# Kernel tuning notes

Measured on AMD Instinct MI355X. Metric: run time of the kernel, lower is better.

Reference implementation:

```python
import jax, jax.numpy as jnp
import numpy as np

B, N, IN_DIM, L_DIM, H_DIM, N_CLASSES, FLOW_LEN = 128, 512, 128, 64, 64, 10, 4


def setup_inputs() -> dict:
    key = jax.random.key(0)
    ks = jax.random.split(key, 20)
    s = 0.05
    return {
        "gs": jax.random.uniform(ks[0], (B, N, N), dtype=jnp.float32),
        "hs": jax.random.normal(ks[1], (B, N, IN_DIM), dtype=jnp.float32),
        "labels": jax.random.randint(ks[2], (B,), 0, N_CLASSES),
        "eps": jax.random.normal(ks[3], (B, N, 1), dtype=jnp.float32),
        "W_s": jax.random.normal(ks[4], (IN_DIM, L_DIM), dtype=jnp.float32) * s,
        "b_s": jnp.zeros((L_DIM,), jnp.float32),
        "W_mu": jax.random.normal(ks[5], (L_DIM, 1), dtype=jnp.float32) * s,
        "b_mu": jnp.zeros((1,), jnp.float32),
        "W_lv": jax.random.normal(ks[6], (L_DIM, 1), dtype=jnp.float32) * s,
        "b_lv": jnp.zeros((1,), jnp.float32),
        "W_dec": jax.random.normal(ks[7], (1, L_DIM), dtype=jnp.float32) * s,
        "b_dec": jnp.zeros((L_DIM,), jnp.float32),
        "W1": jax.random.normal(ks[8], (L_DIM, H_DIM), dtype=jnp.float32) * s,
        "b1": jnp.zeros((H_DIM,), jnp.float32),
        "W2": jax.random.normal(ks[9], (H_DIM, N_CLASSES), dtype=jnp.float32) * s,
        "b2": jnp.zeros((N_CLASSES,), jnp.float32),
        "beta": jax.random.uniform(ks[10], (1,), jnp.float32, 0.0, 100.0),
        "fw": jax.random.normal(ks[11], (FLOW_LEN,), dtype=jnp.float32) * 0.1,
        "fb": jax.random.normal(ks[12], (FLOW_LEN,), dtype=jnp.float32) * 0.1,
        "fs": jax.random.normal(ks[13], (FLOW_LEN,), dtype=jnp.float32) * 0.1,
    }


def reference(gs, hs, labels, eps, W_s, b_s, W_mu, b_mu, W_lv, b_lv,
              W_dec, b_dec, W1, b1, W2, b2, beta, fw, fb, fs):
    relu = jax.nn.relu
    # norm_g: g / g.sum(1) (torch broadcast divides column j by row-sum deg[j])
    deg = gs.sum(axis=2)                       # [B, N]
    g = gs / deg[:, None, :]                   # [B, N, N]

    def gcn(g, h, W, b):
        return relu(jnp.einsum('bij,bjf->bif', g, h) @ W + b)

    h = gcn(g, hs, W_s, b_s)                   # [B, N, L]
    r = h
    mu = gcn(g, h, W_mu, b_mu)                 # [B, N, 1]
    logvar = gcn(g, h, W_lv, b_lv)             # [B, N, 1]
    sigma = jnp.exp(0.5 * logvar)
    z0 = eps * sigma + mu                      # reparameterize (training)

    # 4-step planar flow on scalar latent; log-det accumulated on pre-transform z
    z = z0
    log_jac = jnp.zeros_like(z0)
    for k in range(FLOW_LEN):
        t = jnp.tanh(fw[k] * z + fb[k])
        det = 1.0 + fs[k] * fw[k] * (1.0 - t * t)
        log_jac = log_jac + jnp.log(jnp.abs(det) + 1e-7)
        z = z + fs[k] * t
    zk = z

    # KL = log q(z0) - log_jac - log p(zk), loggaussian = -0.5*((z-mu)/s)^2 - log(2.5 s)
    logq = -0.5 * ((z0 - mu) / sigma) ** 2 - jnp.log(2.5 * sigma)
    logp = -0.5 * zk ** 2 - jnp.log(jnp.float32(2.5))
    kl = logq - log_jac - logp                 # [B, N, 1]

    zs = jax.nn.sigmoid(beta * zk)             # [B, N, 1]
    d = gcn(g, zs, W_dec, b_dec)               # [B, N, L]
    hg = jnp.einsum('bnl,bn->bl', h, zs[..., 0])  # h.T @ zk, [B, L]

    # classify
    x = relu(hg @ W1 + b1)
    logits = jax.nn.log_softmax(x @ W2 + b2, axis=1)  # [B, C]

    nll = -jnp.mean(logits[jnp.arange(B), labels])
    mse = jnp.mean((r - d) ** 2)
    loss = nll + mse + kl.mean()
    preds = jnp.argmax(logits, axis=1)
    acc = jnp.mean((preds == labels).astype(jnp.float32))
    return jnp.stack([loss, acc])
```

## Files before the change

### kernel.cpp

```cpp
#include <hip/hip_runtime.h>
#include <hip/hip_bf16.h>

#define BB 128
#define NN 512
#define IND 128
#define LD 64
#define NC 10
#define FL 4
#define ROWS (BB*NN)
#define HALF 256

#define OFF_ACC 0
#define OFF_RDEG (OFF_ACC + 8)
#define OFF_VM   (OFF_RDEG + ROWS)
#define OFF_VV   (OFF_VM + ROWS)
#define OFF_ZS   (OFF_VV + ROWS)
#define OFF_ZSS  (OFF_ZS + ROWS)
#define OFF_XHG  (OFF_ZSS + ROWS)
#define OFF_H    (OFF_XHG + BB*128)
#define OFF_GSB  (OFF_H + ROWS*32)
#define WS_NEED ((size_t)(OFF_GSB + (size_t)ROWS*256) * 4)

typedef __attribute__((ext_vector_type(8))) short short8v;
typedef __attribute__((ext_vector_type(4))) float f32x4;

__device__ inline float wave_reduce(float v) {
    #pragma unroll
    for (int m = 32; m; m >>= 1) v += __shfl_xor(v, m, 64);
    return v;
}

__device__ inline short f2bf(float f) {
    unsigned u = __float_as_uint(f);
    u += 0x7fff + ((u >> 16) & 1);
    return (short)(u >> 16);
}

__device__ inline float bf2f(short s) {
    return __uint_as_float(((unsigned)(unsigned short)s) << 16);
}

__global__ __launch_bounds__(256) void k_deg(const float* __restrict__ gs,
                                             float* __restrict__ rdeg,
                                             float* __restrict__ accums,
                                             unsigned short* __restrict__ gsb) {
    if (blockIdx.x == 0 && threadIdx.x < 8) accums[threadIdx.x] = 0.f;
    int t = threadIdx.x;
    int row = blockIdx.x * 4 + (t >> 6), lane = t & 63;
    const float4* r4 = (const float4*)(gs + (size_t)row * NN) + lane * 2;
    float4 a = r4[0], b = r4[1];
    float s = a.x + a.y + a.z + a.w + b.x + b.y + b.z + b.w;
    float sr = wave_reduce(s);
    if (lane == 0) rdeg[row] = 1.0f / sr;
    if (gsb) {
        short8v v;
        v[0] = f2bf(a.x); v[1] = f2bf(a.y); v[2] = f2bf(a.z); v[3] = f2bf(a.w);
        v[4] = f2bf(b.x); v[5] = f2bf(b.y); v[6] = f2bf(b.z); v[7] = f2bf(b.w);
        *(short8v*)(gsb + (size_t)row * NN + lane * 8) = v;
    }
}

template<bool BF>
__global__ __launch_bounds__(1024) void k_hwgemm(
    const float* __restrict__ gs, const unsigned short* __restrict__ gsb,
    const float* __restrict__ hs, const float* __restrict__ W_s,
    const float* __restrict__ b_s, const float* __restrict__ W_mu,
    const float* __restrict__ W_lv, const float* __restrict__ rdeg_ws,
    unsigned short* __restrict__ h_ws, float* __restrict__ vm_ws,
    float* __restrict__ vv_ws)
{
    __shared__ unsigned short s_hwT[64 * 512];
    __shared__ unsigned short s_h[HALF * 64];
    __shared__ float s_rdeg[NN];

    const int tid = threadIdx.x, lane = tid & 63, wid = tid >> 6;
    const int b = blockIdx.x >> 1, p = blockIdx.x & 1, rbase = p * HALF;

    if (tid < NN) s_rdeg[tid] = rdeg_ws[(size_t)b * NN + tid];

    unsigned short* sWT = s_h;
    {
        const float4* wp = (const float4*)W_s + tid * 2;
        float4 w0 = wp[0], w1 = wp[1];
        int k = tid >> 3, l0 = (tid & 7) * 8;
        float wv[8] = {w0.x, w0.y, w0.z, w0.w, w1.x, w1.y, w1.z, w1.w};
        #pragma unroll
        for (int e = 0; e < 8; ++e) {
            int l = l0 + e;
            int byte = (l * 256 + k * 2) ^ ((l & 7) << 4);
            *(unsigned short*)((char*)sWT + byte) = (unsigned short)f2bf(wv[e]);
        }
    }
    __syncthreads();

    {
        int n0 = wid * 32, cq = lane & 15, koq = lane >> 4;
        f32x4 accB[2][4] = {};
        #pragma unroll
        for (int kk = 0; kk < 4; ++kk) {
            short8v bf[4];
            #pragma unroll
            for (int lt = 0; lt < 4; ++lt) {
                int l = lt * 16 + cq;
                int byte = (l * 256 + (kk * 32 + koq * 8) * 2) ^ ((l & 7) << 4);
                bf[lt] = *(const short8v*)((char*)sWT + byte);
            }
            #pragma unroll
            for (int nt = 0; nt < 2; ++nt) {
                int row = n0 + nt * 16 + cq;
                const float4* hp = (const float4*)(hs + ((size_t)b * NN + row) * IND
                                                   + kk * 32 + koq * 8);
                float4 h0 = hp[0], h1 = hp[1];
                short8v a;
                a[0] = f2bf(h0.x); a[1] = f2bf(h0.y); a[2] = f2bf(h0.z); a[3] = f2bf(h0.w);
                a[4] = f2bf(h1.x); a[5] = f2bf(h1.y); a[6] = f2bf(h1.z); a[7] = f2bf(h1.w);
                #pragma unroll
                for (int lt = 0; lt < 4; ++lt)
                    accB[nt][lt] = __builtin_amdgcn_mfma_f32_16x16x32_bf16(a, bf[lt], accB[nt][lt], 0, 0, 0);
            }
        }
        __syncthreads();
        int r0 = (lane >> 4) * 4;
        #pragma unroll
        for (int nt = 0; nt < 2; ++nt)
            #pragma unroll
            for (int lt = 0; lt < 4; ++lt)
                #pragma unroll
                for (int q = 0; q < 4; ++q) {
                    int n = n0 + nt * 16 + r0 + q;
                    int l = lt * 16 + cq;
                    int byte = (l * 1024 + n * 2) ^ ((l & 7) << 4);
                    *(unsigned short*)((char*)s_hwT + byte) =
                        (unsigned short)f2bf(accB[nt][lt][q] * s_rdeg[n]);
                }
    }
    __syncthreads();

    {
        int cq = lane & 15, koq = lane >> 4;
        int rowl = wid * 16 + cq, rowg = rbase + rowl;
        const unsigned short* A16 = gsb + ((size_t)b * NN + rowg) * NN + koq * 8;
        const float* A32 = gs + ((size_t)b * NN + rowg) * NN + koq * 8;
        f32x4 accC[4] = {};
        for (int kk = 0; kk < 16; ++kk) {
            short8v bf[4];
            #pragma unroll
            for (int lt = 0; lt < 4; ++lt) {
                int l = lt * 16 + cq;
                int byte = (l * 1024 + (kk * 32 + koq * 8) * 2) ^ ((l & 7) << 4);
                bf[lt] = *(const short8v*)((char*)s_hwT + byte);
            }
            short8v a;
            if constexpr (BF) {
                a = *(const short8v*)(A16 + kk * 32);
            } else {
                const float4* gp = (const float4*)(A32 + kk * 32);
                float4 g0 = gp[0], g1 = gp[1];
                a[0] = f2bf(g0.x); a[1] = f2bf(g0.y); a[2] = f2bf(g0.z); a[3] = f2bf(g0.w);
                a[4] = f2bf(g1.x); a[5] = f2bf(g1.y); a[6] = f2bf(g1.z); a[7] = f2bf(g1.w);
            }
            #pragma unroll
            for (int lt = 0; lt < 4; ++lt)
                accC[lt] = __builtin_amdgcn_mfma_f32_16x16x32_bf16(a, bf[lt], accC[lt], 0, 0, 0);
        }
        int r0 = (lane >> 4) * 4;
        float bsv[4];
        #pragma unroll
        for (int lt = 0; lt < 4; ++lt) bsv[lt] = b_s[lt * 16 + cq];
        #pragma unroll
        for (int lt = 0; lt < 4; ++lt)
            #pragma unroll
            for (int q = 0; q < 4; ++q) {
                int nloc = wid * 16 + r0 + q;
                int l = lt * 16 + cq;
                s_h[nloc * 64 + l] = (unsigned short)f2bf(fmaxf(accC[lt][q] + bsv[lt], 0.f));
            }
    }
    __syncthreads();

    {
        int rowl = tid >> 2, off = (tid & 3) * 16;
        unsigned short* dst = h_ws + ((size_t)(b * NN + rbase + rowl)) * 64 + off;
        const unsigned short* src = &s_h[rowl * 64 + off];
        *(short8v*)dst = *(const short8v*)src;
        *(short8v*)(dst + 8) = *(const short8v*)(src + 8);
    }

    {
        int g16 = tid >> 4, l16 = tid & 15;
        float wmu[4], wlv[4];
        #pragma unroll
        for (int e = 0; e < 4; ++e) { wmu[e] = W_mu[l16 * 4 + e]; wlv[e] = W_lv[l16 * 4 + e]; }
        #pragma unroll
        for (int rr = 0; rr < 4; ++rr) {
            int rowl = g16 * 4 + rr;
            const unsigned short* hp = &s_h[rowl * 64 + l16 * 4];
            float pm = 0.f, pv = 0.f;
            #pragma unroll
            for (int e = 0; e < 4; ++e) {
                float hv = bf2f((short)hp[e]);
                pm += hv * wmu[e]; pv += hv * wlv[e];
            }
            #pragma unroll
            for (int m = 1; m <= 8; m <<= 1) {
                pm += __shfl_xor(pm, m, 64);
                pv += __shfl_xor(pv, m, 64);
            }
            if (l16 == 0) {
                float rd = s_rdeg[rbase + rowl];
                vm_ws[(size_t)b * NN + rbase + rowl] = pm * rd;
                vv_ws[(size_t)b * NN + rbase + rowl] = pv * rd;
            }
        }
    }
}

template<bool BF>
__global__ __launch_bounds__(1024) void k_muflow(
    const float* __restrict__ gs, const unsigned short* __restrict__ gsb,
    const float* __restrict__ vm_ws, const float* __restrict__ vv_ws,
    const float* __restrict__ eps, const float* __restrict__ b_mu,
    const float* __restrict__ b_lv, const float* __restrict__ beta,
    const float* __restrict__ fw, const float* __restrict__ fb,
    const float* __restrict__ fs, const float* __restrict__ rdeg_ws,
    float* __restrict__ zs_ws, float* __restrict__ zss_ws,
    float* __restrict__ accums)
{
    __shared__ float s_mp[HALF], s_lp[HALF];
    __shared__ float s_fin[16];
    const int tid = threadIdx.x, lane = tid & 63, wid = tid >> 6;
    const int b = blockIdx.x >> 1, p = blockIdx.x & 1, rbase = p * HALF;

    float vmr[8], vvr[8];
    #pragma unroll
    for (int e = 0; e < 8; ++e) {
        vmr[e] = vm_ws[(size_t)b * NN + lane * 8 + e];
        vvr[e] = vv_ws[(size_t)b * NN + lane * 8 + e];
    }
    for (int r = 0; r < 16; ++r) {
        int rowl = wid * 16 + r, rowg = rbase + rowl;
        float sm, sv;
        if constexpr (BF) {
            short8v g8 = *(const short8v*)(gsb + ((size_t)b * NN + rowg) * NN + lane * 8);
            float g0 = bf2f(g8[0]), g1 = bf2f(g8[1]), g2 = bf2f(g8[2]), g3 = bf2f(g8[3]);
            float g4 = bf2f(g8[4]), g5 = bf2f(g8[5]), g6 = bf2f(g8[6]), g7 = bf2f(g8[7]);
            sm = g0*vmr[0]+g1*vmr[1]+g2*vmr[2]+g3*vmr[3]+g4*vmr[4]+g5*vmr[5]+g6*vmr[6]+g7*vmr[7];
            sv = g0*vvr[0]+g1*vvr[1]+g2*vvr[2]+g3*vvr[3]+g4*vvr[4]+g5*vvr[5]+g6*vvr[6]+g7*vvr[7];
        } else {
            const float4* gp = (const float4*)(gs + ((size_t)b * NN + rowg) * NN) + lane * 2;
            float4 ga = gp[0], gc = gp[1];
            sm = ga.x*vmr[0]+ga.y*vmr[1]+ga.z*vmr[2]+ga.w*vmr[3]
               + gc.x*vmr[4]+gc.y*vmr[5]+gc.z*vmr[6]+gc.w*vmr[7];
            sv = ga.x*vvr[0]+ga.y*vvr[1]+ga.z*vvr[2]+ga.w*vvr[3]
               + gc.x*vvr[4]+gc.y*vvr[5]+gc.z*vvr[6]+gc.w*vvr[7];
        }
        sm = wave_reduce(sm);
        sv = wave_reduce(sv);
        if (lane == 0) { s_mp[rowl] = sm; s_lp[rowl] = sv; }
    }
    __syncthreads();

    float my_kl = 0.f;
    if (tid < HALF) {
        int rowg = rbase + tid;
        float mu = fmaxf(s_mp[tid] + b_mu[0], 0.f);
        float lv = fmaxf(s_lp[tid] + b_lv[0], 0.f);
        float sigma = expf(0.5f * lv);
        float z0 = eps[(size_t)b * NN + rowg] * sigma + mu;
        float z = z0, lj = 0.f;
        #pragma unroll
        for (int k = 0; k < FL; ++k) {
            float tt = tanhf(fw[k] * z + fb[k]);
            float det = 1.f + fs[k] * fw[k] * (1.f - tt * tt);
            lj += logf(fabsf(det) + 1e-7f);
            z += fs[k] * tt;
        }
        float e0 = (z0 - mu) / sigma;
        float logq = -0.5f * e0 * e0 - logf(2.5f * sigma);
        float logp = -0.5f * z * z - logf(2.5f);
        my_kl = logq - lj - logp;
        float zv = 1.f / (1.f + expf(-beta[0] * z));
        float rd = rdeg_ws[(size_t)b * NN + rowg];
        zs_ws[(size_t)b * NN + rowg] = zv;
        zss_ws[(size_t)b * NN + rowg] = zv * rd;
    }
    float kv = wave_reduce(my_kl);
    if (lane == 0) s_fin[wid] = kv;
    __syncthreads();
    if (tid == 0) {
        float ks = 0.f;
        #pragma unroll
        for (int w = 0; w < 16; ++w) ks += s_fin[w];
        atomicAdd(&accums[0], ks);
    }
}

template<bool BF>
__global__ __launch_bounds__(1024) void k_dec(
    const float* __restrict__ gs, const unsigned short* __restrict__ gsb,
    const float* __restrict__ zss_ws, const float* __restrict__ zs_ws,
    const unsigned short* __restrict__ h_ws, const float* __restrict__ W_dec,
    const float* __restrict__ b_dec, float* __restrict__ accums,
    float* __restrict__ xhg)
{
    __shared__ float s_zs[HALF];
    __shared__ float s_red[16 * 68];
    __shared__ float s_fin[16];
    const int tid = threadIdx.x, lane = tid & 63, wid = tid >> 6;
    const int b = blockIdx.x >> 1, p = blockIdx.x & 1, rbase = p * HALF;

    if (tid < HALF) s_zs[tid] = zs_ws[(size_t)b * NN + rbase + tid];
    float zr[8];
    #pragma unroll
    for (int e = 0; e < 8; ++e) zr[e] = zss_ws[(size_t)b * NN + lane * 8 + e];
    float wd = W_dec[lane], bd = b_dec[lane];
    __syncthreads();

    float msacc = 0.f, hgacc = 0.f;
    for (int r = 0; r < 16; ++r) {
        int rowl = wid * 16 + r, rowg = rbase + rowl;
        float s;
        if constexpr (BF) {
            short8v g8 = *(const short8v*)(gsb + ((size_t)b * NN + rowg) * NN + lane * 8);
            s = bf2f(g8[0])*zr[0]+bf2f(g8[1])*zr[1]+bf2f(g8[2])*zr[2]+bf2f(g8[3])*zr[3]
              + bf2f(g8[4])*zr[4]+bf2f(g8[5])*zr[5]+bf2f(g8[6])*zr[6]+bf2f(g8[7])*zr[7];
        } else {
            const float4* gp = (const float4*)(gs + ((size_t)b * NN + rowg) * NN) + lane * 2;
            float4 ga = gp[0], gc = gp[1];
            s = ga.x*zr[0]+ga.y*zr[1]+ga.z*zr[2]+ga.w*zr[3]
              + gc.x*zr[4]+gc.y*zr[5]+gc.z*zr[6]+gc.w*zr[7];
        }
        s = wave_reduce(s);
        float dval = fmaxf(s * wd + bd, 0.f);
        float hval = bf2f((short)h_ws[((size_t)b * NN + rowg) * 64 + lane]);
        float diff = hval - dval;
        msacc += diff * diff;
        hgacc += hval * s_zs[rowl];
    }
    s_red[wid * 68 + lane] = hgacc;
    float mv = wave_reduce(msacc);
    if (lane == 0) s_fin[wid] = mv;
    __syncthreads();
    if (tid == 0) {
        float ms = 0.f;
        #pragma unroll
        for (int w = 0; w < 16; ++w) ms += s_fin[w];
        atomicAdd(&accums[1], ms);
    }
    if (wid == 0) {
        float hgv = 0.f;
        #pragma unroll
        for (int w = 0; w < 16; ++w) hgv += s_red[w * 68 + lane];
        xhg[(size_t)b * 128 + p * 64 + lane] = hgv;
    }
}

__global__ __launch_bounds__(64) void k_cls(const float* __restrict__ xhg,
                                            const float* __restrict__ W1,
                                            const float* __restrict__ b1,
                                            const float* __restrict__ W2,
                                            const float* __restrict__ b2,
                                            const int* __restrict__ labels,
                                            float* __restrict__ accums,
                                            float* __restrict__ out)
{
    __shared__ float s_hg[64], s_x[64], s_lg[12];
    int b = blockIdx.x, l = threadIdx.x;
    s_hg[l] = xhg[(size_t)b * 128 + l] + xhg[(size_t)b * 128 + 64 + l];
    __syncthreads();
    float x = b1[l];
    #pragma unroll 8
    for (int k = 0; k < LD; ++k) x += s_hg[k] * W1[k * LD + l];
    s_x[l] = fmaxf(x, 0.f);
    __syncthreads();
    if (l < NC) {
        float lg = b2[l];
        #pragma unroll 8
        for (int k = 0; k < LD; ++k) lg += s_x[k] * W2[k * NC + l];
        s_lg[l] = lg;
    }
    __syncthreads();
    if (l == 0) {
        float mx = s_lg[0]; int pred = 0;
        #pragma unroll
        for (int c = 1; c < NC; ++c) if (s_lg[c] > mx) { mx = s_lg[c]; pred = c; }
        float se = 0.f;
        #pragma unroll
        for (int c = 0; c < NC; ++c) se += expf(s_lg[c] - mx);
        int lab = labels[b];
        atomicAdd(&accums[2], -(s_lg[lab] - (mx + logf(se))));
        if (pred == lab) atomicAdd(&accums[3], 1.0f);
        __threadfence();
        unsigned old = atomicAdd((unsigned*)&accums[4], 1u);
        if (old == BB - 1) {
            float kk = atomicAdd(&accums[0], 0.f);
            float mm = atomicAdd(&accums[1], 0.f);
            float nn = atomicAdd(&accums[2], 0.f);
            float aa = atomicAdd(&accums[3], 0.f);
            out[0] = nn / (float)BB
                   + mm / ((float)BB * NN * LD)
                   + kk / ((float)BB * NN);
            out[1] = aa / (float)BB;
        }
    }
}

extern "C" void kernel_launch(void* const* d_in, const int* in_sizes, int n_in,
                              void* d_out, int out_size, void* d_ws, size_t ws_size,
                              hipStream_t stream) {
    const float* gs    = (const float*)d_in[0];
    const float* hs    = (const float*)d_in[1];
    const int*   labels= (const int*)d_in[2];
    const float* eps   = (const float*)d_in[3];
    const float* W_s   = (const float*)d_in[4];
    const float* b_s   = (const float*)d_in[5];
    const float* W_mu  = (const float*)d_in[6];
    const float* b_mu  = (const float*)d_in[7];
    const float* W_lv  = (const float*)d_in[8];
    const float* b_lv  = (const float*)d_in[9];
    const float* W_dec = (const float*)d_in[10];
    const float* b_dec = (const float*)d_in[11];
    const float* W1    = (const float*)d_in[12];
    const float* b1    = (const float*)d_in[13];
    const float* W2    = (const float*)d_in[14];
    const float* b2    = (const float*)d_in[15];
    const float* beta  = (const float*)d_in[16];
    const float* fw    = (const float*)d_in[17];
    const float* fb    = (const float*)d_in[18];
    const float* fs    = (const float*)d_in[19];

    float* ws      = (float*)d_ws;
    float* accums  = ws + OFF_ACC;
    float* rdeg    = ws + OFF_RDEG;
    float* vm_ws   = ws + OFF_VM;
    float* vv_ws   = ws + OFF_VV;
    float* zs_ws   = ws + OFF_ZS;
    float* zss_ws  = ws + OFF_ZSS;
    float* xhg     = ws + OFF_XHG;
    unsigned short* h_ws = (unsigned short*)(ws + OFF_H);
    unsigned short* gsb  = (unsigned short*)(ws + OFF_GSB);
    float* out = (float*)d_out;

    bool big = ws_size >= WS_NEED;

    k_deg<<<ROWS / 4, 256, 0, stream>>>(gs, rdeg, accums, big ? gsb : nullptr);
    if (big) {
        k_hwgemm<true><<<2 * BB, 1024, 0, stream>>>(gs, gsb, hs, W_s, b_s, W_mu, W_lv,
                                                    rdeg, h_ws, vm_ws, vv_ws);
        k_muflow<true><<<2 * BB, 1024, 0, stream>>>(gs, gsb, vm_ws, vv_ws, eps, b_mu, b_lv,
                                                    beta, fw, fb, fs, rdeg, zs_ws, zss_ws,
                                                    accums);
        k_dec<true><<<2 * BB, 1024, 0, stream>>>(gs, gsb, zss_ws, zs_ws, h_ws, W_dec, b_dec,
                                                 accums, xhg);
    } else {
        k_hwgemm<false><<<2 * BB, 1024, 0, stream>>>(gs, gsb, hs, W_s, b_s, W_mu, W_lv,
                                                     rdeg, h_ws, vm_ws, vv_ws);
        k_muflow<false><<<2 * BB, 1024, 0, stream>>>(gs, gsb, vm_ws, vv_ws, eps, b_mu, b_lv,
                                                     beta, fw, fb, fs, rdeg, zs_ws, zss_ws,
                                                     accums);
        k_dec<false><<<2 * BB, 1024, 0, stream>>>(gs, gsb, zss_ws, zs_ws, h_ws, W_dec, b_dec,
                                                  accums, xhg);
    }
    k_cls<<<BB, 64, 0, stream>>>(xhg, W1, b1, W2, b2, labels, accums, out);
}
```

Measured before the change: 103.6 us.

## Use bf16 MFMA for mu/logvar and decoder matvecs, split rows into quarters

Replaces the per-row wave-reduced scalar dot products in k_muflow and k_dec with 16x16x32 bf16 MFMA instructions. The vector operands are converted to bf16 and staged in shared memory. Grid goes from 2 to 4 blocks per graph with 512 threads each. Per-block atomics for KL and MSE become per-block partial writes that k_cls sums. This removes the shuffle-reduction cost and adds parallelism, but it rounds the vectors to bf16 and wastes most MFMA columns because they are zero-padded.

```diff
diff --git a/kernel.cpp b/kernel.cpp
--- a/kernel.cpp
+++ b/kernel.cpp
@@ -9,6 +9,7 @@
 #define FL 4
 #define ROWS (BB*NN)
 #define HALF 256
+#define QTR 128
 
 #define OFF_ACC 0
 #define OFF_RDEG (OFF_ACC + 8)
@@ -16,8 +17,10 @@
 #define OFF_VV   (OFF_VM + ROWS)
 #define OFF_ZS   (OFF_VV + ROWS)
 #define OFF_ZSS  (OFF_ZS + ROWS)
-#define OFF_XHG  (OFF_ZSS + ROWS)
-#define OFF_H    (OFF_XHG + BB*128)
+#define OFF_KLP  (OFF_ZSS + ROWS)
+#define OFF_MSEP (OFF_KLP + 512)
+#define OFF_XHG  (OFF_MSEP + 512)
+#define OFF_H    (OFF_XHG + BB*256)
 #define OFF_GSB  (OFF_H + ROWS*32)
 #define WS_NEED ((size_t)(OFF_GSB + (size_t)ROWS*256) * 4)
 
@@ -216,7 +219,7 @@
 }
 
 template<bool BF>
-__global__ __launch_bounds__(1024) void k_muflow(
+__global__ __launch_bounds__(512) void k_muflow(
     const float* __restrict__ gs, const unsigned short* __restrict__ gsb,
     const float* __restrict__ vm_ws, const float* __restrict__ vv_ws,
     const float* __restrict__ eps, const float* __restrict__ b_mu,
@@ -224,49 +227,59 @@
     const float* __restrict__ fw, const float* __restrict__ fb,
     const float* __restrict__ fs, const float* __restrict__ rdeg_ws,
     float* __restrict__ zs_ws, float* __restrict__ zss_ws,
-    float* __restrict__ accums)
+    float* __restrict__ klp)
 {
-    __shared__ float s_mp[HALF], s_lp[HALF];
-    __shared__ float s_fin[16];
+    __shared__ unsigned short s_bmu[NN], s_blv[NN];
+    __shared__ float s_mp[QTR], s_lp[QTR];
+    __shared__ float s_fin[8];
     const int tid = threadIdx.x, lane = tid & 63, wid = tid >> 6;
-    const int b = blockIdx.x >> 1, p = blockIdx.x & 1, rbase = p * HALF;
-
-    float vmr[8], vvr[8];
-    #pragma unroll
-    for (int e = 0; e < 8; ++e) {
-        vmr[e] = vm_ws[(size_t)b * NN + lane * 8 + e];
-        vvr[e] = vv_ws[(size_t)b * NN + lane * 8 + e];
-    }
-    for (int r = 0; r < 16; ++r) {
-        int rowl = wid * 16 + r, rowg = rbase + rowl;
-        float sm, sv;
+    const int b = blockIdx.x >> 2, qb = blockIdx.x & 3, rbase = qb * QTR;
+
+    if (tid < NN) {
+        s_bmu[tid] = (unsigned short)f2bf(vm_ws[(size_t)b * NN + tid]);
+        s_blv[tid] = (unsigned short)f2bf(vv_ws[(size_t)b * NN + tid]);
+    }
+    __syncthreads();
+
+    const int cq = lane & 15, koq = lane >> 4;
+    const int rowl = wid * 16 + cq, rowg = rbase + rowl;
+    const unsigned short* A16 = gsb + ((size_t)b * NN + rowg) * NN + koq * 8;
+    const float* A32 = gs + ((size_t)b * NN + rowg) * NN + koq * 8;
+    const char* bptr = (cq == 1) ? (const char*)s_blv : (const char*)s_bmu;
+    f32x4 acc = {0.f, 0.f, 0.f, 0.f};
+    const short8v bz = {0, 0, 0, 0, 0, 0, 0, 0};
+    #pragma unroll 4
+    for (int kk = 0; kk < 16; ++kk) {
+        short8v a;
         if constexpr (BF) {
-            short8v g8 = *(const short8v*)(gsb + ((size_t)b * NN + rowg) * NN + lane * 8);
-            float g0 = bf2f(g8[0]), g1 = bf2f(g8[1]), g2 = bf2f(g8[2]), g3 = bf2f(g8[3]);
-            float g4 = bf2f(g8[4]), g5 = bf2f(g8[5]), g6 = bf2f(g8[6]), g7 = bf2f(g8[7]);
-            sm = g0*vmr[0]+g1*vmr[1]+g2*vmr[2]+g3*vmr[3]+g4*vmr[4]+g5*vmr[5]+g6*vmr[6]+g7*vmr[7];
-            sv = g0*vvr[0]+g1*vvr[1]+g2*vvr[2]+g3*vvr[3]+g4*vvr[4]+g5*vvr[5]+g6*vvr[6]+g7*vvr[7];
+            a = *(const short8v*)(A16 + kk * 32);
         } else {
-            const float4* gp = (const float4*)(gs + ((size_t)b * NN + rowg) * NN) + lane * 2;
-            float4 ga = gp[0], gc = gp[1];
-            sm = ga.x*vmr[0]+ga.y*vmr[1]+ga.z*vmr[2]+ga.w*vmr[3]
-               + gc.x*vmr[4]+gc.y*vmr[5]+gc.z*vmr[6]+gc.w*vmr[7];
-            sv = ga.x*vvr[0]+ga.y*vvr[1]+ga.z*vvr[2]+ga.w*vvr[3]
-               + gc.x*vvr[4]+gc.y*vvr[5]+gc.z*vvr[6]+gc.w*vvr[7];
-        }
-        sm = wave_reduce(sm);
-        sv = wave_reduce(sv);
-        if (lane == 0) { s_mp[rowl] = sm; s_lp[rowl] = sv; }
+            const float4* gp = (const float4*)(A32 + kk * 32);
+            float4 g0 = gp[0], g1 = gp[1];
+            a[0] = f2bf(g0.x); a[1] = f2bf(g0.y); a[2] = f2bf(g0.z); a[3] = f2bf(g0.w);
+            a[4] = f2bf(g1.x); a[5] = f2bf(g1.y); a[6] = f2bf(g1.z); a[7] = f2bf(g1.w);
+        }
+        short8v bl = *(const short8v*)(bptr + (kk * 32 + koq * 8) * 2);
+        short8v bfrag = (cq < 2) ? bl : bz;
+        acc = __builtin_amdgcn_mfma_f32_16x16x32_bf16(a, bfrag, acc, 0, 0, 0);
+    }
+    int r0 = (lane >> 4) * 4;
+    if (cq == 0) {
+        #pragma unroll
+        for (int q2 = 0; q2 < 4; ++q2) s_mp[wid * 16 + r0 + q2] = acc[q2];
+    } else if (cq == 1) {
+        #pragma unroll
+        for (int q2 = 0; q2 < 4; ++q2) s_lp[wid * 16 + r0 + q2] = acc[q2];
     }
     __syncthreads();
 
     float my_kl = 0.f;
-    if (tid < HALF) {
-        int rowg = rbase + tid;
+    if (tid < QTR) {
+        int rg = rbase + tid;
         float mu = fmaxf(s_mp[tid] + b_mu[0], 0.f);
         float lv = fmaxf(s_lp[tid] + b_lv[0], 0.f);
         float sigma = expf(0.5f * lv);
-        float z0 = eps[(size_t)b * NN + rowg] * sigma + mu;
+        float z0 = eps[(size_t)b * NN + rg] * sigma + mu;
         float z = z0, lj = 0.f;
         #pragma unroll
         for (int k = 0; k < FL; ++k) {
@@ -280,9 +293,9 @@
         float logp = -0.5f * z * z - logf(2.5f);
         my_kl = logq - lj - logp;
         float zv = 1.f / (1.f + expf(-beta[0] * z));
-        float rd = rdeg_ws[(size_t)b * NN + rowg];
-        zs_ws[(size_t)b * NN + rowg] = zv;
-        zss_ws[(size_t)b * NN + rowg] = zv * rd;
+        float rd = rdeg_ws[(size_t)b * NN + rg];
+        zs_ws[(size_t)b * NN + rg] = zv;
+        zss_ws[(size_t)b * NN + rg] = zv * rd;
     }
     float kv = wave_reduce(my_kl);
     if (lane == 0) s_fin[wid] = kv;
@@ -290,52 +303,69 @@
     if (tid == 0) {
         float ks = 0.f;
         #pragma unroll
-        for (int w = 0; w < 16; ++w) ks += s_fin[w];
-        atomicAdd(&accums[0], ks);
+        for (int w = 0; w < 8; ++w) ks += s_fin[w];
+        klp[blockIdx.x] = ks;
     }
 }
 
 template<bool BF>
-__global__ __launch_bounds__(1024) void k_dec(
+__global__ __launch_bounds__(512) void k_dec(
     const float* __restrict__ gs, const unsigned short* __restrict__ gsb,
     const float* __restrict__ zss_ws, const float* __restrict__ zs_ws,
     const unsigned short* __restrict__ h_ws, const float* __restrict__ W_dec,
-    const float* __restrict__ b_dec, float* __restrict__ accums,
+    const float* __restrict__ b_dec, float* __restrict__ msep,
     float* __restrict__ xhg)
 {
-    __shared__ float s_zs[HALF];
-    __shared__ float s_red[16 * 68];
-    __shared__ float s_fin[16];
+    __shared__ unsigned short s_bz[NN];
+    __shared__ float s_zs[QTR];
+    __shared__ float s_dp[QTR];
+    __shared__ float s_red[8 * 68];
+    __shared__ float s_fin[8];
     const int tid = threadIdx.x, lane = tid & 63, wid = tid >> 6;
-    const int b = blockIdx.x >> 1, p = blockIdx.x & 1, rbase = p * HALF;
-
-    if (tid < HALF) s_zs[tid] = zs_ws[(size_t)b * NN + rbase + tid];
-    float zr[8];
-    #pragma unroll
-    for (int e = 0; e < 8; ++e) zr[e] = zss_ws[(size_t)b * NN + lane * 8 + e];
+    const int b = blockIdx.x >> 2, qb = blockIdx.x & 3, rbase = qb * QTR;
+
+    if (tid < NN) s_bz[tid] = (unsigned short)f2bf(zss_ws[(size_t)b * NN + tid]);
+    if (tid < QTR) s_zs[tid] = zs_ws[(size_t)b * NN + rbase + tid];
+    __syncthreads();
+
+    const int cq = lane & 15, koq = lane >> 4;
+    const int rowl = wid * 16 + cq, rowg = rbase + rowl;
+    const unsigned short* A16 = gsb + ((size_t)b * NN + rowg) * NN + koq * 8;
+    const float* A32 = gs + ((size_t)b * NN + rowg) * NN + koq * 8;
+    f32x4 acc = {0.f, 0.f, 0.f, 0.f};
+    const short8v bz = {0, 0, 0, 0, 0, 0, 0, 0};
+    #pragma unroll 4
+    for (int kk = 0; kk < 16; ++kk) {
+        short8v a;
+        if constexpr (BF) {
+            a = *(const short8v*)(A16 + kk * 32);
+        } else {
+            const float4* gp = (const float4*)(A32 + kk * 32);
+            float4 g0 = gp[0], g1 = gp[1];
+            a[0] = f2bf(g0.x); a[1] = f2bf(g0.y); a[2] = f2bf(g0.z); a[3] = f2bf(g0.w);
+            a[4] = f2bf(g1.x); a[5] = f2bf(g1.y); a[6] = f2bf(g1.z); a[7] = f2bf(g1.w);
+        }
+        short8v bl = *(const short8v*)((const char*)s_bz + (kk * 32 + koq * 8) * 2);
+        short8v bfrag = (cq == 0) ? bl : bz;
+        acc = __builtin_amdgcn_mfma_f32_16x16x32_bf16(a, bfrag, acc, 0, 0, 0);
+    }
+    int r0 = (lane >> 4) * 4;
+    if (cq == 0) {
+        #pragma unroll
+        for (int q2 = 0; q2 < 4; ++q2) s_dp[wid * 16 + r0 + q2] = acc[q2];
+    }
+    __syncthreads();
+
     float wd = W_dec[lane], bd = b_dec[lane];
-    __syncthreads();
-
     float msacc = 0.f, hgacc = 0.f;
+    #pragma unroll 4
     for (int r = 0; r < 16; ++r) {
-        int rowl = wid * 16 + r, rowg = rbase + rowl;
-        float s;
-        if constexpr (BF) {
-            short8v g8 = *(const short8v*)(gsb + ((size_t)b * NN + rowg) * NN + lane * 8);
-            s = bf2f(g8[0])*zr[0]+bf2f(g8[1])*zr[1]+bf2f(g8[2])*zr[2]+bf2f(g8[3])*zr[3]
-              + bf2f(g8[4])*zr[4]+bf2f(g8[5])*zr[5]+bf2f(g8[6])*zr[6]+bf2f(g8[7])*zr[7];
-        } else {
-            const float4* gp = (const float4*)(gs + ((size_t)b * NN + rowg) * NN) + lane * 2;
-            float4 ga = gp[0], gc = gp[1];
-            s = ga.x*zr[0]+ga.y*zr[1]+ga.z*zr[2]+ga.w*zr[3]
-              + gc.x*zr[4]+gc.y*zr[5]+gc.z*zr[6]+gc.w*zr[7];
-        }
-        s = wave_reduce(s);
-        float dval = fmaxf(s * wd + bd, 0.f);
-        float hval = bf2f((short)h_ws[((size_t)b * NN + rowg) * 64 + lane]);
+        int rl = wid * 16 + r, rg = rbase + rl;
+        float dval = fmaxf(s_dp[rl] * wd + bd, 0.f);
+        float hval = bf2f((short)h_ws[((size_t)b * NN + rg) * 64 + lane]);
         float diff = hval - dval;
         msacc += diff * diff;
-        hgacc += hval * s_zs[rowl];
+        hgacc += hval * s_zs[rl];
     }
     s_red[wid * 68 + lane] = hgacc;
     float mv = wave_reduce(msacc);
@@ -344,18 +374,20 @@
     if (tid == 0) {
         float ms = 0.f;
         #pragma unroll
-        for (int w = 0; w < 16; ++w) ms += s_fin[w];
-        atomicAdd(&accums[1], ms);
+        for (int w = 0; w < 8; ++w) ms += s_fin[w];
+        msep[blockIdx.x] = ms;
     }
     if (wid == 0) {
         float hgv = 0.f;
         #pragma unroll
-        for (int w = 0; w < 16; ++w) hgv += s_red[w * 68 + lane];
-        xhg[(size_t)b * 128 + p * 64 + lane] = hgv;
+        for (int w = 0; w < 8; ++w) hgv += s_red[w * 68 + lane];
+        xhg[(size_t)b * 256 + qb * 64 + lane] = hgv;
     }
 }
 
 __global__ __launch_bounds__(64) void k_cls(const float* __restrict__ xhg,
+                                            const float* __restrict__ klp,
+                                            const float* __restrict__ msep,
                                             const float* __restrict__ W1,
                                             const float* __restrict__ b1,
                                             const float* __restrict__ W2,
@@ -366,7 +398,10 @@
 {
     __shared__ float s_hg[64], s_x[64], s_lg[12];
     int b = blockIdx.x, l = threadIdx.x;
-    s_hg[l] = xhg[(size_t)b * 128 + l] + xhg[(size_t)b * 128 + 64 + l];
+    s_hg[l] = xhg[(size_t)b * 256 + l] + xhg[(size_t)b * 256 + 64 + l]
+            + xhg[(size_t)b * 256 + 128 + l] + xhg[(size_t)b * 256 + 192 + l];
+    if (l == 0) atomicAdd(&accums[0], klp[4*b] + klp[4*b+1] + klp[4*b+2] + klp[4*b+3]);
+    if (l == 1) atomicAdd(&accums[1], msep[4*b] + msep[4*b+1] + msep[4*b+2] + msep[4*b+3]);
     __syncthreads();
     float x = b1[l];
     #pragma unroll 8
@@ -436,6 +471,8 @@
     float* vv_ws   = ws + OFF_VV;
     float* zs_ws   = ws + OFF_ZS;
     float* zss_ws  = ws + OFF_ZSS;
+    float* klp     = ws + OFF_KLP;
+    float* msep    = ws + OFF_MSEP;
     float* xhg     = ws + OFF_XHG;
     unsigned short* h_ws = (unsigned short*)(ws + OFF_H);
     unsigned short* gsb  = (unsigned short*)(ws + OFF_GSB);
@@ -447,19 +484,19 @@
     if (big) {
         k_hwgemm<true><<<2 * BB, 1024, 0, stream>>>(gs, gsb, hs, W_s, b_s, W_mu, W_lv,
                                                     rdeg, h_ws, vm_ws, vv_ws);
-        k_muflow<true><<<2 * BB, 1024, 0, stream>>>(gs, gsb, vm_ws, vv_ws, eps, b_mu, b_lv,
-                                                    beta, fw, fb, fs, rdeg, zs_ws, zss_ws,
-                                                    accums);
-        k_dec<true><<<2 * BB, 1024, 0, stream>>>(gs, gsb, zss_ws, zs_ws, h_ws, W_dec, b_dec,
-                                                 accums, xhg);
+        k_muflow<true><<<4 * BB, 512, 0, stream>>>(gs, gsb, vm_ws, vv_ws, eps, b_mu, b_lv,
+                                                   beta, fw, fb, fs, rdeg, zs_ws, zss_ws,
+                                                   klp);
+        k_dec<true><<<4 * BB, 512, 0, stream>>>(gs, gsb, zss_ws, zs_ws, h_ws, W_dec, b_dec,
+                                                msep, xhg);
     } else {
         k_hwgemm<false><<<2 * BB, 1024, 0, stream>>>(gs, gsb, hs, W_s, b_s, W_mu, W_lv,
                                                      rdeg, h_ws, vm_ws, vv_ws);
-        k_muflow<false><<<2 * BB, 1024, 0, stream>>>(gs, gsb, vm_ws, vv_ws, eps, b_mu, b_lv,
-                                                     beta, fw, fb, fs, rdeg, zs_ws, zss_ws,
-                                                     accums);
-        k_dec<false><<<2 * BB, 1024, 0, stream>>>(gs, gsb, zss_ws, zs_ws, h_ws, W_dec, b_dec,
-                                                  accums, xhg);
-    }
-    k_cls<<<BB, 64, 0, stream>>>(xhg, W1, b1, W2, b2, labels, accums, out);
-}
+        k_muflow<false><<<4 * BB, 512, 0, stream>>>(gs, gsb, vm_ws, vv_ws, eps, b_mu, b_lv,
+                                                    beta, fw, fb, fs, rdeg, zs_ws, zss_ws,
+                                                    klp);
+        k_dec<false><<<4 * BB, 512, 0, stream>>>(gs, gsb, zss_ws, zs_ws, h_ws, W_dec, b_dec,
+                                                 msep, xhg);
+    }
+    k_cls<<<BB, 64, 0, stream>>>(xhg, klp, msep, W1, b1, W2, b2, labels, accums, out);
+}
```

After: 101.9 us, median of 2. About the same (-1.7%).
